# Optimization experiments

Hardware: AMD Instinct MI355X
Metric: run time of the kernel (lower is better)

Reference implementation:

```python
import jax, jax.numpy as jnp
import numpy as np

N = 10000
E = 320000
F_IN = 256
HID = 256
C_OUT = 40
NUM_BASES = 10
NUM_REL = 2


def _rgcn_layer(x, edge_index, edge_type, basis, comp, root, bias):
    # basis: [B, d_in, d_out], comp: [R, B] -> per-relation weights [R, d_in, d_out]
    W = jnp.einsum('rb,bio->rio', comp, basis)
    src, dst = edge_index[0], edge_index[1]
    n = x.shape[0]
    out = x @ root + bias  # self/root transform
    xg = x[src]  # [E, d_in] gathered source features
    for r in range(NUM_REL):  # fixed small relation count
        m = (edge_type == r).astype(x.dtype)  # [E]
        msg = (xg @ W[r]) * m[:, None]  # [E, d_out]
        s = jax.ops.segment_sum(msg, dst, num_segments=n)
        cnt = jax.ops.segment_sum(m, dst, num_segments=n)
        out = out + s / jnp.maximum(cnt, 1.0)[:, None]  # mean aggregation (PyG RGCNConv default)
    return out


def setup_inputs() -> dict:
    key = jax.random.key(0)
    ks = jax.random.split(key, 16)
    inp = {
        'x': jax.random.normal(ks[0], (N, F_IN), dtype=jnp.float32),
        'edge_index': jax.random.randint(ks[1], (2, E), 0, N, dtype=jnp.int64),
        'edge_type': jax.random.randint(ks[2], (E,), 0, NUM_REL, dtype=jnp.int64),
    }
    dims = [(F_IN, HID), (HID, HID), (HID, C_OUT)]
    for i, (di, do) in enumerate(dims, start=1):
        s = 1.0 / np.sqrt(di)
        inp[f'basis{i}'] = jax.random.normal(ks[3 * i], (NUM_BASES, di, do), dtype=jnp.float32) * s
        inp[f'comp{i}'] = jax.random.normal(ks[3 * i + 1], (NUM_REL, NUM_BASES), dtype=jnp.float32)
        inp[f'root{i}'] = jax.random.normal(ks[3 * i + 2], (di, do), dtype=jnp.float32) * s
        inp[f'bias{i}'] = jnp.zeros((do,), dtype=jnp.float32)
    return inp


def reference(x, edge_index, edge_type,
              basis1, comp1, root1, bias1,
              basis2, comp2, root2, bias2,
              basis3, comp3, root3, bias3):
    # layer 1 + relu (dropout is identity in eval mode)
    x = _rgcn_layer(x, edge_index, edge_type, basis1, comp1, root1, bias1)
    x = jax.nn.relu(x)
    # layer 2 + relu
    x = _rgcn_layer(x, edge_index, edge_type, basis2, comp2, root2, bias2)
    x = jax.nn.relu(x)
    # final layer + log_softmax over classes
    x = _rgcn_layer(x, edge_index, edge_type, basis3, comp3, root3, bias3)
    return jax.nn.log_softmax(x, axis=1)
```

## Files before the change

### kernel.cpp

```cpp
#include <hip/hip_runtime.h>
#include <math.h>

#define NREL 2
#define NB 10
#define C_OUT 40
#define CAP 64

typedef unsigned int u32;
typedef unsigned short u16;
typedef unsigned char u8;
typedef __attribute__((ext_vector_type(8))) short bf16x8;
typedef __attribute__((ext_vector_type(4))) float f32x4;

#define MFMA16 __builtin_amdgcn_mfma_f32_16x16x32_bf16

__device__ __forceinline__ u32 rne16(float v) {
    u32 u = __float_as_uint(v);
    return (u + 0x7FFFu + ((u >> 16) & 1u)) >> 16;
}
__device__ __forceinline__ u32 pack_split(float v) {
    u32 u = __float_as_uint(v);
    u32 hi = (u + 0x7FFFu + ((u >> 16) & 1u)) & 0xFFFF0000u;
    float r = v - __uint_as_float(hi);
    u32 ur = __float_as_uint(r);
    u32 lo = ((ur + 0x7FFFu + ((ur >> 16) & 1u)) >> 16) & 0xFFFFu;
    return hi | lo;
}
__device__ __forceinline__ float bfbits(u32 w) { return __uint_as_float(w); }

__device__ __forceinline__ u32 pk_fp8_pair(float a, float b) {
    return (u32)__builtin_amdgcn_cvt_pk_fp8_f32(a, b, 0, false) & 0xFFFFu;
}
__device__ __forceinline__ u8 fp8_1(float a) {
    return (u8)((u32)__builtin_amdgcn_cvt_pk_fp8_f32(a, a, 0, false) & 0xFFu);
}

__global__ void fused_pre(const float* __restrict__ x, u16* __restrict__ xP,
                          u8* __restrict__ xQ, int* __restrict__ cnt, int M2, int n2) {
    int g = blockIdx.x * 256 + threadIdx.x;
    if (g < M2) cnt[g] = 0;
    if (g >= n2) return;
    int i = g * 2;
    float v0 = x[i], v1 = x[i + 1];
    u32 w = rne16(v0) | (rne16(v1) << 16);
    *(u32*)&xP[i] = w;
    *(u16*)&xQ[i] = (u16)pk_fp8_pair(v0, v1);
}

__global__ void fill_edges_cap(const int* __restrict__ ei, const int* __restrict__ et,
                               int* __restrict__ cnt, int* __restrict__ elist, int E_) {
    int e = blockIdx.x * 256 + threadIdx.x;
    if (e < E_) {
        int src = ei[e];
        int dst = ei[E_ + e];
        int r = et[e];
        int idx = dst * 2 + r;
        int pos = atomicAdd(&cnt[idx], 1);
        if (pos < CAP) elist[idx * CAP + pos] = src;
    }
}

__global__ void build_wt_all(const float* __restrict__ basis1, const float* __restrict__ comp1,
                             const float* __restrict__ root1, u16* __restrict__ Wt1,
                             const float* __restrict__ basis2, const float* __restrict__ comp2,
                             const float* __restrict__ root2, u16* __restrict__ Wt2,
                             const float* __restrict__ basis3, const float* __restrict__ comp3,
                             const float* __restrict__ root3, u16* __restrict__ Wt3) {
    int layer = blockIdx.y;
    const float* basis = (layer == 0) ? basis1 : (layer == 1) ? basis2 : basis3;
    const float* comp = (layer == 0) ? comp1 : (layer == 1) ? comp2 : comp3;
    const float* root = (layer == 0) ? root1 : (layer == 1) ? root2 : root3;
    u16* Wt = (layer == 0) ? Wt1 : (layer == 1) ? Wt2 : Wt3;
    int dreal = (layer == 2) ? C_OUT : 256;
    int dpad = (layer == 2) ? 64 : 256;

    int c = threadIdx.x;
    if (c >= dpad) return;
    int k0 = blockIdx.x * 4;
    float cw[NREL][NB];
#pragma unroll
    for (int r = 0; r < NREL; ++r)
#pragma unroll
        for (int b = 0; b < NB; ++b) cw[r][b] = comp[r * NB + b];
#pragma unroll
    for (int t = 0; t < 4; ++t) {
        int k = k0 + t;
        float v = 0.f;
        if (c < dreal) {
            if (k < 256) {
                v = root[k * dreal + c];
            } else {
                int r = (k - 256) >> 8;
                int i = (k - 256) & 255;
#pragma unroll
                for (int b = 0; b < NB; ++b)
                    v += cw[r][b] * basis[(b * 256 + i) * dreal + c];
            }
        }
        u32 pk = pack_split(v);
        int cb = c >> 4, kc = k >> 5, kg = (k >> 3) & 3, e = k & 7;
        size_t idx = ((size_t)(cb * 24 + kc) * 64 + (kg * 16 + (c & 15))) * 8 + e;
        Wt[idx] = (u16)(pk >> 16);
        if (layer == 2) Wt[(size_t)4 * 24 * 512 + idx] = (u16)(pk & 0xFFFFu);
    }
}

__global__ __launch_bounds__(256) void agg_wave(const u8* __restrict__ hQ,
                                                const int* __restrict__ cnt,
                                                const int* __restrict__ elist,
                                                u16* __restrict__ aggP, int M2) {
    int wid = blockIdx.x * 4 + (threadIdx.x >> 6);
    if (wid >= M2) return;
    int lane = threadIdx.x & 63;
    int half = lane >> 5;
    int fl = (lane & 31) * 8;
    int c = cnt[wid];
    int cc = min(c, CAP);
    const int* ep = elist + (size_t)wid * CAP;

    float s0 = 0.f, s1 = 0.f, s2 = 0.f, s3 = 0.f, s4 = 0.f, s5 = 0.f, s6 = 0.f, s7 = 0.f;

#define ACC8(q)                                            \
    do {                                                   \
        s0 += __builtin_amdgcn_cvt_f32_fp8((q).x, 0);      \
        s1 += __builtin_amdgcn_cvt_f32_fp8((q).x, 1);      \
        s2 += __builtin_amdgcn_cvt_f32_fp8((q).x, 2);      \
        s3 += __builtin_amdgcn_cvt_f32_fp8((q).x, 3);      \
        s4 += __builtin_amdgcn_cvt_f32_fp8((q).y, 0);      \
        s5 += __builtin_amdgcn_cvt_f32_fp8((q).y, 1);      \
        s6 += __builtin_amdgcn_cvt_f32_fp8((q).y, 2);      \
        s7 += __builtin_amdgcn_cvt_f32_fp8((q).y, 3);      \
    } while (0)

    int fullpairs = cc >> 1;
    int jp = 0;
    for (; jp + 3 < fullpairs; jp += 4) {
        int e0 = ep[2 * jp + half];
        int e1 = ep[2 * jp + 2 + half];
        int e2 = ep[2 * jp + 4 + half];
        int e3 = ep[2 * jp + 6 + half];
        uint2 q0 = *(const uint2*)(hQ + (size_t)e0 * 256 + fl);
        uint2 q1 = *(const uint2*)(hQ + (size_t)e1 * 256 + fl);
        uint2 q2 = *(const uint2*)(hQ + (size_t)e2 * 256 + fl);
        uint2 q3 = *(const uint2*)(hQ + (size_t)e3 * 256 + fl);
        ACC8(q0);
        ACC8(q1);
        ACC8(q2);
        ACC8(q3);
    }
    for (; jp < fullpairs; ++jp) {
        int e0 = ep[2 * jp + half];
        uint2 q0 = *(const uint2*)(hQ + (size_t)e0 * 256 + fl);
        ACC8(q0);
    }
    if (cc & 1) {
        int e0 = ep[cc - 1];
        if (half == 0) {
            uint2 q0 = *(const uint2*)(hQ + (size_t)e0 * 256 + fl);
            ACC8(q0);
        }
    }
#undef ACC8

    s0 += __shfl_xor(s0, 32, 64);
    s1 += __shfl_xor(s1, 32, 64);
    s2 += __shfl_xor(s2, 32, 64);
    s3 += __shfl_xor(s3, 32, 64);
    s4 += __shfl_xor(s4, 32, 64);
    s5 += __shfl_xor(s5, 32, 64);
    s6 += __shfl_xor(s6, 32, 64);
    s7 += __shfl_xor(s7, 32, 64);

    if (half == 0) {
        float inv = (c > 0) ? 1.f / (float)c : 0.f;
        uint4 o;
        o.x = rne16(s0 * inv) | (rne16(s1 * inv) << 16);
        o.y = rne16(s2 * inv) | (rne16(s3 * inv) << 16);
        o.z = rne16(s4 * inv) | (rne16(s5 * inv) << 16);
        o.w = rne16(s6 * inv) | (rne16(s7 * inv) << 16);
        int n = wid >> 1, r = wid & 1;
        *(uint4*)&aggP[(size_t)n * 512 + r * 256 + fl] = o;
    }
}

__global__ __launch_bounds__(512) void gemm_mfma_big(
    const u16* __restrict__ A0, const u16* __restrict__ A1,
    const u16* __restrict__ Wf, const float* __restrict__ bias,
    u16* __restrict__ OutP, u8* __restrict__ OutQ, int M) {
    __shared__ u16 ldsA[48 * 512];
    int tid = threadIdx.x;
    int lane = tid & 63;
    int w = tid >> 6;
    int wr = w >> 2, wc = w & 3;
    int l15 = lane & 15, l4 = lane >> 4;
    int rb0 = blockIdx.x * 32;

    {
        uint4 sv[6];
#pragma unroll
        for (int i = 0; i < 6; ++i) {
            int u = i * 8 + w;
            int r16 = (u >= 24) ? 1 : 0;
            int kc = u - r16 * 24;
            int row = rb0 + r16 * 16 + l15;
            const u16* src = (kc < 8) ? A0 + (size_t)row * 256 + kc * 32 + l4 * 8
                                      : A1 + (size_t)row * 512 + (kc - 8) * 32 + l4 * 8;
            sv[i] = *(const uint4*)src;
        }
#pragma unroll
        for (int i = 0; i < 6; ++i) {
            int u = i * 8 + w;
            *(uint4*)&ldsA[(size_t)u * 512 + lane * 8] = sv[i];
        }
    }
    __syncthreads();

    const u16* wbase = Wf + (size_t)wc * 4 * 24 * 512 + lane * 8;
    const u16* abase = ldsA + (size_t)wr * 24 * 512 + lane * 8;
    f32x4 acc[4] = {};
    bf16x8 pa[4], pb[4][4];

    auto LOADC = [&](int c, int s) {
        pa[s] = *(const bf16x8*)&abase[(size_t)c * 512];
#pragma unroll
        for (int ct = 0; ct < 4; ++ct)
            pb[s][ct] = *(const bf16x8*)&wbase[(size_t)(ct * 24 + c) * 512];
    };

    LOADC(0, 0);
    LOADC(1, 1);
    LOADC(2, 2);
#pragma unroll
    for (int c = 0; c < 24; ++c) {
        const int s = c & 3;
        if (c + 3 < 24) LOADC(c + 3, (c + 3) & 3);
#pragma unroll
        for (int ct = 0; ct < 4; ++ct)
            acc[ct] = MFMA16(pa[s], pb[s][ct], acc[ct], 0, 0, 0);
    }

#pragma unroll
    for (int ct = 0; ct < 4; ++ct) {
        int col = wc * 64 + ct * 16 + l15;
        float b = bias[col];
#pragma unroll
        for (int j = 0; j < 4; ++j) {
            int row = rb0 + wr * 16 + l4 * 4 + j;
            if (row < M) {
                float v = fmaxf(acc[ct][j] + b, 0.f);
                OutP[(size_t)row * 256 + col] = (u16)rne16(v);
                OutQ[(size_t)row * 256 + col] = fp8_1(v);
            }
        }
    }
}

__global__ __launch_bounds__(256) void gemm_mfma_small(
    const u16* __restrict__ A0, const u16* __restrict__ A1,
    const u16* __restrict__ Wf, const float* __restrict__ bias,
    float* __restrict__ Out, int M) {
    int tid = threadIdx.x;
    int lane = tid & 63;
    int w = tid >> 6;
    int l15 = lane & 15, l4 = lane >> 4;
    int row0 = blockIdx.x * 64 + w * 16;
    int arow = row0 + l15;

    const u16* a0b = A0 + (size_t)arow * 256 + l4 * 8;
    const u16* a1b = A1 + (size_t)arow * 512 + l4 * 8;
    const u16* wb = Wf + lane * 8;
    const u16* wbl = wb + 4 * 24 * 512;

    f32x4 acc[3] = {};
    bf16x8 pa[2], pbh[2][3], pbl[2][3];

    auto LOADC = [&](int c, int s) {
        pa[s] = (c < 8) ? *(const bf16x8*)(a0b + c * 32)
                        : *(const bf16x8*)(a1b + (c - 8) * 32);
#pragma unroll
        for (int ct = 0; ct < 3; ++ct) {
            pbh[s][ct] = *(const bf16x8*)(wb + (size_t)(ct * 24 + c) * 512);
            pbl[s][ct] = *(const bf16x8*)(wbl + (size_t)(ct * 24 + c) * 512);
        }
    };

    LOADC(0, 0);
#pragma unroll
    for (int c = 0; c < 24; ++c) {
        const int s = c & 1;
        if (c + 1 < 24) LOADC(c + 1, (c + 1) & 1);
#pragma unroll
        for (int ct = 0; ct < 3; ++ct) {
            acc[ct] = MFMA16(pa[s], pbh[s][ct], acc[ct], 0, 0, 0);
            acc[ct] = MFMA16(pa[s], pbl[s][ct], acc[ct], 0, 0, 0);
        }
    }

    bool val2 = (l15 < 8);
    float bq0 = bias[l15];
    float bq1 = bias[16 + l15];
    float bq2 = val2 ? bias[32 + l15] : 0.f;

#pragma unroll
    for (int j = 0; j < 4; ++j) {
        float v0 = acc[0][j] + bq0;
        float v1 = acc[1][j] + bq1;
        float v2 = val2 ? (acc[2][j] + bq2) : -INFINITY;
        float m = fmaxf(fmaxf(v0, v1), v2);
#pragma unroll
        for (int d = 1; d < 16; d <<= 1) m = fmaxf(m, __shfl_xor(m, d, 64));
        float s = expf(v0 - m) + expf(v1 - m) + (val2 ? expf(v2 - m) : 0.f);
#pragma unroll
        for (int d = 1; d < 16; d <<= 1) s += __shfl_xor(s, d, 64);
        float ls = m + logf(s);
        int row = row0 + l4 * 4 + j;
        if (row < M) {
            Out[(size_t)row * C_OUT + l15] = v0 - ls;
            Out[(size_t)row * C_OUT + 16 + l15] = v1 - ls;
            if (val2) Out[(size_t)row * C_OUT + 32 + l15] = v2 - ls;
        }
    }
}

extern "C" void kernel_launch(void* const* d_in, const int* in_sizes, int n_in,
                              void* d_out, int out_size, void* d_ws, size_t ws_size,
                              hipStream_t stream) {
    const float* x = (const float*)d_in[0];
    const int* ei = (const int*)d_in[1];
    const int* et = (const int*)d_in[2];
    const float* basis1 = (const float*)d_in[3];
    const float* comp1 = (const float*)d_in[4];
    const float* root1 = (const float*)d_in[5];
    const float* bias1 = (const float*)d_in[6];
    const float* basis2 = (const float*)d_in[7];
    const float* comp2 = (const float*)d_in[8];
    const float* root2 = (const float*)d_in[9];
    const float* bias2 = (const float*)d_in[10];
    const float* basis3 = (const float*)d_in[11];
    const float* comp3 = (const float*)d_in[12];
    const float* root3 = (const float*)d_in[13];
    const float* bias3 = (const float*)d_in[14];

    int N_ = in_sizes[0] / 256;
    int E_ = in_sizes[2];
    int M2 = 2 * N_;
    int Mpad = (N_ + 63) & ~63;

    char* p = (char*)d_ws;
    size_t o = 0;
    auto alloc = [&](size_t bytes) {
        void* r = p + o;
        o += (bytes + 255) & ~(size_t)255;
        return r;
    };
    int* cnt = (int*)alloc((size_t)M2 * 4);
    int* elist = (int*)alloc((size_t)M2 * CAP * 4);
    u16* Wf1 = (u16*)alloc((size_t)16 * 24 * 512 * 2);
    u16* Wf2 = (u16*)alloc((size_t)16 * 24 * 512 * 2);
    u16* Wf3 = (u16*)alloc((size_t)2 * 4 * 24 * 512 * 2);
    u16* xP = (u16*)alloc((size_t)Mpad * 256 * 2);
    u16* h1P = (u16*)alloc((size_t)Mpad * 256 * 2);
    u16* aggP = (u16*)alloc((size_t)Mpad * 512 * 2);
    u8* xQ = (u8*)alloc((size_t)Mpad * 256);
    u8* h1Q = (u8*)alloc((size_t)Mpad * 256);
    u16* h2P = xP;
    u8* h2Q = xQ;
    (void)ws_size;

    int n2 = N_ * 128;

    fused_pre<<<(n2 + 255) / 256, 256, 0, stream>>>(x, xP, xQ, cnt, M2, n2);
    {
        dim3 g(192, 3);
        build_wt_all<<<g, 256, 0, stream>>>(basis1, comp1, root1, Wf1,
                                            basis2, comp2, root2, Wf2,
                                            basis3, comp3, root3, Wf3);
    }
    fill_edges_cap<<<(E_ + 255) / 256, 256, 0, stream>>>(ei, et, cnt, elist, E_);

    int gblocks = (N_ + 31) / 32;
    int sblocks = (N_ + 63) / 64;
    int ablocks = (M2 + 3) / 4;

    agg_wave<<<ablocks, 256, 0, stream>>>(xQ, cnt, elist, aggP, M2);
    gemm_mfma_big<<<gblocks, 512, 0, stream>>>(xP, aggP, Wf1, bias1, h1P, h1Q, N_);
    agg_wave<<<ablocks, 256, 0, stream>>>(h1Q, cnt, elist, aggP, M2);
    gemm_mfma_big<<<gblocks, 512, 0, stream>>>(h1P, aggP, Wf2, bias2, h2P, h2Q, N_);
    agg_wave<<<ablocks, 256, 0, stream>>>(h2Q, cnt, elist, aggP, M2);
    gemm_mfma_small<<<sblocks, 256, 0, stream>>>(h2P, aggP, Wf3, bias3, (float*)d_out, N_);
}
```

Measured before the change: 137.5 us.

## Fuse neighbor aggregation into the per-layer MFMA GEMM via LDS

Each layer's separate aggregation kernel and GEMM kernel are merged into one kernel. Each 512-thread block gathers and mean-reduces neighbor fp8 features for its 32 nodes straight into the LDS A-tile, then runs the MFMA GEMM. This removes the aggP round trip through global memory and three kernel launches. In exchange, gather latency is no longer overlapped across a separate grid, fewer waves hide gather latency per block, and the small final layer now uses only 2 of 8 waves for its GEMM.

```diff
diff --git a/kernel.cpp b/kernel.cpp
--- a/kernel.cpp
+++ b/kernel.cpp
@@ -26,13 +26,22 @@
     u32 lo = ((ur + 0x7FFFu + ((ur >> 16) & 1u)) >> 16) & 0xFFFFu;
     return hi | lo;
 }
-__device__ __forceinline__ float bfbits(u32 w) { return __uint_as_float(w); }
 
 __device__ __forceinline__ u32 pk_fp8_pair(float a, float b) {
     return (u32)__builtin_amdgcn_cvt_pk_fp8_f32(a, b, 0, false) & 0xFFFFu;
 }
 __device__ __forceinline__ u8 fp8_1(float a) {
     return (u8)((u32)__builtin_amdgcn_cvt_pk_fp8_f32(a, a, 0, false) & 0xFFu);
+}
+__device__ __forceinline__ void acc8(float* s, uint2 q) {
+    s[0] += __builtin_amdgcn_cvt_f32_fp8(q.x, 0);
+    s[1] += __builtin_amdgcn_cvt_f32_fp8(q.x, 1);
+    s[2] += __builtin_amdgcn_cvt_f32_fp8(q.x, 2);
+    s[3] += __builtin_amdgcn_cvt_f32_fp8(q.x, 3);
+    s[4] += __builtin_amdgcn_cvt_f32_fp8(q.y, 0);
+    s[5] += __builtin_amdgcn_cvt_f32_fp8(q.y, 1);
+    s[6] += __builtin_amdgcn_cvt_f32_fp8(q.y, 2);
+    s[7] += __builtin_amdgcn_cvt_f32_fp8(q.y, 3);
 }
 
 __global__ void fused_pre(const float* __restrict__ x, u16* __restrict__ xP,
@@ -105,32 +114,17 @@
     }
 }
 
-__global__ __launch_bounds__(256) void agg_wave(const u8* __restrict__ hQ,
-                                                const int* __restrict__ cnt,
-                                                const int* __restrict__ elist,
-                                                u16* __restrict__ aggP, int M2) {
-    int wid = blockIdx.x * 4 + (threadIdx.x >> 6);
-    if (wid >= M2) return;
-    int lane = threadIdx.x & 63;
+__device__ __forceinline__ void gather_unit(const u8* __restrict__ hQ,
+                                            const int* __restrict__ elist,
+                                            u16* ldsA, int node, int rel, int c,
+                                            int nodeofs, int lane) {
     int half = lane >> 5;
-    int fl = (lane & 31) * 8;
-    int c = cnt[wid];
+    int q = lane & 31;
+    int fl = q * 8;
     int cc = min(c, CAP);
-    const int* ep = elist + (size_t)wid * CAP;
-
-    float s0 = 0.f, s1 = 0.f, s2 = 0.f, s3 = 0.f, s4 = 0.f, s5 = 0.f, s6 = 0.f, s7 = 0.f;
-
-#define ACC8(q)                                            \
-    do {                                                   \
-        s0 += __builtin_amdgcn_cvt_f32_fp8((q).x, 0);      \
-        s1 += __builtin_amdgcn_cvt_f32_fp8((q).x, 1);      \
-        s2 += __builtin_amdgcn_cvt_f32_fp8((q).x, 2);      \
-        s3 += __builtin_amdgcn_cvt_f32_fp8((q).x, 3);      \
-        s4 += __builtin_amdgcn_cvt_f32_fp8((q).y, 0);      \
-        s5 += __builtin_amdgcn_cvt_f32_fp8((q).y, 1);      \
-        s6 += __builtin_amdgcn_cvt_f32_fp8((q).y, 2);      \
-        s7 += __builtin_amdgcn_cvt_f32_fp8((q).y, 3);      \
-    } while (0)
+    const int* ep = elist + (size_t)(node * 2 + rel) * CAP;
+
+    float s[8] = {0.f, 0.f, 0.f, 0.f, 0.f, 0.f, 0.f, 0.f};
 
     int fullpairs = cc >> 1;
     int jp = 0;
@@ -143,48 +137,43 @@
         uint2 q1 = *(const uint2*)(hQ + (size_t)e1 * 256 + fl);
         uint2 q2 = *(const uint2*)(hQ + (size_t)e2 * 256 + fl);
         uint2 q3 = *(const uint2*)(hQ + (size_t)e3 * 256 + fl);
-        ACC8(q0);
-        ACC8(q1);
-        ACC8(q2);
-        ACC8(q3);
+        acc8(s, q0);
+        acc8(s, q1);
+        acc8(s, q2);
+        acc8(s, q3);
     }
     for (; jp < fullpairs; ++jp) {
         int e0 = ep[2 * jp + half];
         uint2 q0 = *(const uint2*)(hQ + (size_t)e0 * 256 + fl);
-        ACC8(q0);
+        acc8(s, q0);
     }
     if (cc & 1) {
         int e0 = ep[cc - 1];
         if (half == 0) {
             uint2 q0 = *(const uint2*)(hQ + (size_t)e0 * 256 + fl);
-            ACC8(q0);
-        }
-    }
-#undef ACC8
-
-    s0 += __shfl_xor(s0, 32, 64);
-    s1 += __shfl_xor(s1, 32, 64);
-    s2 += __shfl_xor(s2, 32, 64);
-    s3 += __shfl_xor(s3, 32, 64);
-    s4 += __shfl_xor(s4, 32, 64);
-    s5 += __shfl_xor(s5, 32, 64);
-    s6 += __shfl_xor(s6, 32, 64);
-    s7 += __shfl_xor(s7, 32, 64);
+            acc8(s, q0);
+        }
+    }
+
+#pragma unroll
+    for (int j = 0; j < 8; ++j) s[j] += __shfl_xor(s[j], 32, 64);
 
     if (half == 0) {
         float inv = (c > 0) ? 1.f / (float)c : 0.f;
         uint4 o;
-        o.x = rne16(s0 * inv) | (rne16(s1 * inv) << 16);
-        o.y = rne16(s2 * inv) | (rne16(s3 * inv) << 16);
-        o.z = rne16(s4 * inv) | (rne16(s5 * inv) << 16);
-        o.w = rne16(s6 * inv) | (rne16(s7 * inv) << 16);
-        int n = wid >> 1, r = wid & 1;
-        *(uint4*)&aggP[(size_t)n * 512 + r * 256 + fl] = o;
-    }
-}
-
-__global__ __launch_bounds__(512) void gemm_mfma_big(
-    const u16* __restrict__ A0, const u16* __restrict__ A1,
+        o.x = rne16(s[0] * inv) | (rne16(s[1] * inv) << 16);
+        o.y = rne16(s[2] * inv) | (rne16(s[3] * inv) << 16);
+        o.z = rne16(s[4] * inv) | (rne16(s[5] * inv) << 16);
+        o.w = rne16(s[6] * inv) | (rne16(s[7] * inv) << 16);
+        int r16 = nodeofs >> 4, l15r = nodeofs & 15;
+        int kc = 8 + rel * 8 + (q >> 2), kg = q & 3;
+        *(uint4*)&ldsA[(size_t)(r16 * 24 + kc) * 512 + (kg * 16 + l15r) * 8] = o;
+    }
+}
+
+__global__ __launch_bounds__(512) void fused_layer_big(
+    const u16* __restrict__ hP, const u8* __restrict__ hQ,
+    const int* __restrict__ cnt, const int* __restrict__ elist,
     const u16* __restrict__ Wf, const float* __restrict__ bias,
     u16* __restrict__ OutP, u8* __restrict__ OutQ, int M) {
     __shared__ u16 ldsA[48 * 512];
@@ -195,22 +184,31 @@
     int l15 = lane & 15, l4 = lane >> 4;
     int rb0 = blockIdx.x * 32;
 
+#pragma unroll
+    for (int i = 0; i < 2; ++i) {
+        int idx = w * 2 + i;
+        int u = (idx < 8) ? idx : idx + 16;
+        int r16 = (u >= 24) ? 1 : 0;
+        int kc = u - r16 * 24;
+        int row = rb0 + r16 * 16 + l15;
+        uint4 v = *(const uint4*)(hP + (size_t)row * 256 + kc * 32 + l4 * 8);
+        *(uint4*)&ldsA[(size_t)u * 512 + lane * 8] = v;
+    }
+
     {
-        uint4 sv[6];
-#pragma unroll
-        for (int i = 0; i < 6; ++i) {
-            int u = i * 8 + w;
-            int r16 = (u >= 24) ? 1 : 0;
-            int kc = u - r16 * 24;
-            int row = rb0 + r16 * 16 + l15;
-            const u16* src = (kc < 8) ? A0 + (size_t)row * 256 + kc * 32 + l4 * 8
-                                      : A1 + (size_t)row * 512 + (kc - 8) * 32 + l4 * 8;
-            sv[i] = *(const uint4*)src;
-        }
-#pragma unroll
-        for (int i = 0; i < 6; ++i) {
-            int u = i * 8 + w;
-            *(uint4*)&ldsA[(size_t)u * 512 + lane * 8] = sv[i];
+        int cw8[8];
+#pragma unroll
+        for (int i = 0; i < 8; ++i) {
+            int g = w * 8 + i;
+            int node = rb0 + (g >> 1);
+            cw8[i] = (node < M) ? cnt[node * 2 + (g & 1)] : 0;
+        }
+        for (int i = 0; i < 8; ++i) {
+            int g = w * 8 + i;
+            int nodeofs = g >> 1, rel = g & 1;
+            int node = rb0 + nodeofs;
+            if (node < M)
+                gather_unit(hQ, elist, ldsA, node, rel, cw8[i], nodeofs, lane);
         }
     }
     __syncthreads();
@@ -255,19 +253,52 @@
     }
 }
 
-__global__ __launch_bounds__(256) void gemm_mfma_small(
-    const u16* __restrict__ A0, const u16* __restrict__ A1,
+__global__ __launch_bounds__(512) void fused_layer_small(
+    const u16* __restrict__ hP, const u8* __restrict__ hQ,
+    const int* __restrict__ cnt, const int* __restrict__ elist,
     const u16* __restrict__ Wf, const float* __restrict__ bias,
     float* __restrict__ Out, int M) {
+    __shared__ u16 ldsA[48 * 512];
     int tid = threadIdx.x;
     int lane = tid & 63;
     int w = tid >> 6;
     int l15 = lane & 15, l4 = lane >> 4;
-    int row0 = blockIdx.x * 64 + w * 16;
-    int arow = row0 + l15;
-
-    const u16* a0b = A0 + (size_t)arow * 256 + l4 * 8;
-    const u16* a1b = A1 + (size_t)arow * 512 + l4 * 8;
+    int rb0 = blockIdx.x * 32;
+
+#pragma unroll
+    for (int i = 0; i < 2; ++i) {
+        int idx = w * 2 + i;
+        int u = (idx < 8) ? idx : idx + 16;
+        int r16 = (u >= 24) ? 1 : 0;
+        int kc = u - r16 * 24;
+        int row = rb0 + r16 * 16 + l15;
+        uint4 v = *(const uint4*)(hP + (size_t)row * 256 + kc * 32 + l4 * 8);
+        *(uint4*)&ldsA[(size_t)u * 512 + lane * 8] = v;
+    }
+
+    {
+        int cw8[8];
+#pragma unroll
+        for (int i = 0; i < 8; ++i) {
+            int g = w * 8 + i;
+            int node = rb0 + (g >> 1);
+            cw8[i] = (node < M) ? cnt[node * 2 + (g & 1)] : 0;
+        }
+        for (int i = 0; i < 8; ++i) {
+            int g = w * 8 + i;
+            int nodeofs = g >> 1, rel = g & 1;
+            int node = rb0 + nodeofs;
+            if (node < M)
+                gather_unit(hQ, elist, ldsA, node, rel, cw8[i], nodeofs, lane);
+        }
+    }
+    __syncthreads();
+
+    if (w >= 2) return;
+    int wr = w;
+    int row0 = rb0 + wr * 16;
+
+    const u16* abase = ldsA + (size_t)wr * 24 * 512 + lane * 8;
     const u16* wb = Wf + lane * 8;
     const u16* wbl = wb + 4 * 24 * 512;
 
@@ -275,8 +306,7 @@
     bf16x8 pa[2], pbh[2][3], pbl[2][3];
 
     auto LOADC = [&](int c, int s) {
-        pa[s] = (c < 8) ? *(const bf16x8*)(a0b + c * 32)
-                        : *(const bf16x8*)(a1b + (c - 8) * 32);
+        pa[s] = *(const bf16x8*)&abase[(size_t)c * 512];
 #pragma unroll
         for (int ct = 0; ct < 3; ++ct) {
             pbh[s][ct] = *(const bf16x8*)(wb + (size_t)(ct * 24 + c) * 512);
@@ -360,7 +390,6 @@
     u16* Wf3 = (u16*)alloc((size_t)2 * 4 * 24 * 512 * 2);
     u16* xP = (u16*)alloc((size_t)Mpad * 256 * 2);
     u16* h1P = (u16*)alloc((size_t)Mpad * 256 * 2);
-    u16* aggP = (u16*)alloc((size_t)Mpad * 512 * 2);
     u8* xQ = (u8*)alloc((size_t)Mpad * 256);
     u8* h1Q = (u8*)alloc((size_t)Mpad * 256);
     u16* h2P = xP;
@@ -379,13 +408,11 @@
     fill_edges_cap<<<(E_ + 255) / 256, 256, 0, stream>>>(ei, et, cnt, elist, E_);
 
     int gblocks = (N_ + 31) / 32;
-    int sblocks = (N_ + 63) / 64;
-    int ablocks = (M2 + 3) / 4;
-
-    agg_wave<<<ablocks, 256, 0, stream>>>(xQ, cnt, elist, aggP, M2);
-    gemm_mfma_big<<<gblocks, 512, 0, stream>>>(xP, aggP, Wf1, bias1, h1P, h1Q, N_);
-    agg_wave<<<ablocks, 256, 0, stream>>>(h1Q, cnt, elist, aggP, M2);
-    gemm_mfma_big<<<gblocks, 512, 0, stream>>>(h1P, aggP, Wf2, bias2, h2P, h2Q, N_);
-    agg_wave<<<ablocks, 256, 0, stream>>>(h2Q, cnt, elist, aggP, M2);
-    gemm_mfma_small<<<sblocks, 256, 0, stream>>>(h2P, aggP, Wf3, bias3, (float*)d_out, N_);
-}
+
+    fused_layer_big<<<gblocks, 512, 0, stream>>>(xP, xQ, cnt, elist, Wf1, bias1,
+                                                 h1P, h1Q, N_);
+    fused_layer_big<<<gblocks, 512, 0, stream>>>(h1P, h1Q, cnt, elist, Wf2, bias2,
+                                                 h2P, h2Q, N_);
+    fused_layer_small<<<gblocks, 512, 0, stream>>>(h2P, h2Q, cnt, elist, Wf3, bias3,
+                                                   (float*)d_out, N_);
+}
```

After: 150.5 us. +9.4%, slower.
